# Kernel optimization log

Hardware: AMD Instinct MI355X
Metric: run time of the kernel (lower is better)

The kernel has to match this reference:

```python
import jax, jax.numpy as jnp
import numpy as np


def _apply_ring(x, angles):
    """Apply x @ R^T where R = G_0 @ G_1 @ ... @ G_{n-1} with ring planes
    (k, (k+1) % n). Equivalent to applying G_k^T to x for k = n-1 .. 0:
      x[:, k] <- c*x[:, k] - s*x[:, j]
      x[:, j] <- s*x[:, k] + c*x[:, j]
    x: [B, n], angles: [n].
    """
    n = angles.shape[0]

    def step(xT, k):
        a = angles[k]
        c, s = jnp.cos(a), jnp.sin(a)
        j = jnp.mod(k + 1, n)
        xi = xT[k]
        xj = xT[j]
        xT = xT.at[k].set(c * xi - s * xj)
        xT = xT.at[j].set(s * xi + c * xj)
        return xT, None

    ks = jnp.arange(n - 1, -1, -1)  # reverse order: R^T = G_{n-1}^T ... G_0^T
    xT, _ = jax.lax.scan(step, x.T, ks)  # carry is [n, B]
    return xT.T


def setup_inputs() -> dict:
    key = jax.random.key(0)
    k_x, k_e, k_d = jax.random.split(key, 3)
    B, n, num_blocks = 8192, 1024, 4
    return {
        "x": jax.random.normal(k_x, (B, n), dtype=jnp.float32),
        "angles_enc": jax.random.normal(k_e, (num_blocks, n), dtype=jnp.float32),
        "angles_dec": jax.random.normal(k_d, (num_blocks, n), dtype=jnp.float32),
        "hidden_weight": jnp.zeros((1,), dtype=jnp.float32),
        "hidden_state": jnp.zeros((n,), dtype=jnp.float32),
    }


def reference(x, angles_enc, angles_dec, hidden_weight, hidden_state):
    num_blocks = angles_enc.shape[0]
    b = x
    for blk in range(num_blocks):
        b = _apply_ring(b, angles_enc[blk])
    # recurrent blend; weight uses the detached hidden_weight (original uses
    # numpy on .detach()), so stop_gradient matches the original semantics.
    w = jax.nn.sigmoid(jax.lax.stop_gradient(hidden_weight[0]))
    bottleneck = (1.0 - w) * b + w * hidden_state[None, :]
    out = bottleneck
    for blk in range(num_blocks):
        out = _apply_ring(out, angles_dec[blk])
    return (bottleneck, out)
```

## Files before the change

kernel.cpp:

```cpp
#include <hip/hip_runtime.h>
#include <math.h>

#define N_COLS 1024
#define NRINGS 8

#define TPR    32
#define CHUNK  32
#define ROWS_PER_BLOCK 8

#define F_OFF   16384
#define A_OFF   24576
#define AUX_OFF 24832
#define WS_FLOATS 24848

__global__ __launch_bounds__(256)
void ced_setup(const float* __restrict__ ae,
               const float* __restrict__ ad,
               float* __restrict__ ws)
{
    __shared__ float2 ls[N_COLS];
    const int r   = blockIdx.x;
    const int tid = threadIdx.x;
    const float* ang = (r < 4) ? (ae + (r << 10)) : (ad + ((r - 4) << 10));

    #pragma unroll
    for (int m = 0; m < 4; ++m) {
        int k = (m << 8) + tid;
        float sv, cv;
        sincosf(ang[k], &sv, &cv);
        if (k == N_COLS - 1) {
            ((float2*)(ws + AUX_OFF))[r] = make_float2(cv, sv);
            cv = 0.f; sv = -1.f;
        }
        ls[k] = make_float2(cv, sv);
    }
    __syncthreads();

    const int t = tid >> 3;
    const int q = tid & 7;
    const int j0 = t * CHUNK + 4 * q;
    float2 e0 = ls[j0], e1 = ls[j0+1], e2 = ls[j0+2], e3 = ls[j0+3];

    float4* CSw = (float4*)ws;
    CSw[(r*16 + 2*q    )*32 + t] = make_float4(e0.x, e0.y, e1.x, e1.y);
    CSw[(r*16 + 2*q + 1)*32 + t] = make_float4(e2.x, e2.y, e3.x, e3.y);

    float f3 = e3.x;       float P = -e3.y;
    float f2 = e2.x * P;   P *= -e2.y;
    float f1 = e1.x * P;   P *= -e1.y;
    float f0 = e0.x * P;   P *= -e0.y;

    float ip = P;
    #pragma unroll
    for (int d = 1; d < 8; d <<= 1) {
        float tmp = __shfl_down(ip, d);
        if (q + d < 8) ip *= tmp;
    }
    float ex = __shfl_down(ip, 1);
    if (q == 7) ex = 1.f;
    f0 *= ex; f1 *= ex; f2 *= ex; f3 *= ex;

    float4* Fw = (float4*)(ws + F_OFF);
    Fw[(r*8 + q)*32 + t] = make_float4(f0, f1, f2, f3);
    if (q == 0) ws[A_OFF + r*TPR + t] = ip;
}

__global__ __launch_bounds__(256, 4)
void ced_main(const float* __restrict__ x,
              const float* __restrict__ ws,
              const float* __restrict__ hw,
              const float* __restrict__ hs,
              float* __restrict__ out, int B)
{
    const float4* CS  = (const float4*)ws;
    const float4* F   = (const float4*)(ws + F_OFF);
    const float*  A   = ws + A_OFF;
    const float2* AUX = (const float2*)(ws + AUX_OFF);

    const int tid  = threadIdx.x;
    const int lane = tid & 63;
    const int t    = lane & 31;
    const int g    = lane >> 5;
    const int groupBase = lane & 32;
    const int row  = blockIdx.x * ROWS_PER_BLOCK + (tid >> 6) * 2 + g;

    float y[CHUNK];
    const float4* xp = (const float4*)(x + (size_t)row * N_COLS + t * CHUNK);
    #pragma unroll
    for (int i = 0; i < 8; ++i) {
        float4 v = xp[i];
        y[4*i] = v.x; y[4*i+1] = v.y; y[4*i+2] = v.z; y[4*i+3] = v.w;
    }

    const float w   = 1.f / (1.f + expf(-hw[0]));
    const float omw = 1.f - w;

    #pragma unroll 1
    for (int r = 0; r < NRINGS; ++r) {
        if (r == 4) {
            float4* ob = (float4*)(out + (size_t)row * N_COLS + t * CHUNK);
            const float4* hp = (const float4*)(hs + t * CHUNK);
            #pragma unroll
            for (int i = 0; i < 8; ++i) {
                float4 h = hp[i];
                float4 bn;
                bn.x = fmaf(omw, y[4*i+0], w * h.x);
                bn.y = fmaf(omw, y[4*i+1], w * h.y);
                bn.z = fmaf(omw, y[4*i+2], w * h.z);
                bn.w = fmaf(omw, y[4*i+3], w * h.w);
                ob[i] = bn;
                y[4*i+0] = bn.x; y[4*i+1] = bn.y; y[4*i+2] = bn.z; y[4*i+3] = bn.w;
            }
        }

        const float4* csr = CS + r * 512 + t;
        float4 cs_all[16];
        #pragma unroll
        for (int jp = 0; jp < 16; ++jp) cs_all[jp] = csr[jp * 32];

        const float2 cN = AUX[r];
        float y0 = __shfl(y[0],       groupBase);
        float yN = __shfl(y[CHUNK-1], groupBase + 31);
        float Cinit = cN.x * yN - cN.y * y0;
        float x0n   = fmaf(cN.y, yN, cN.x * y0);
        if (t == 0) y[0] = x0n;

        float carry = 0.f, ztmp = 0.f;
        #pragma unroll
        for (int jp = CHUNK/2 - 1; jp >= 0; --jp) {
            float4 cs4 = cs_all[jp];
            const int j1 = 2*jp + 1;
            float z1 = fmaf(cs4.w, y[j1], cs4.z * carry);
            carry    = fmaf(-cs4.w, carry, cs4.z * y[j1]);
            if (j1 == CHUNK - 1) ztmp = z1; else y[j1+1] = z1;
            const int j0 = 2*jp;
            float z0s = fmaf(cs4.y, y[j0], cs4.x * carry);
            carry     = fmaf(-cs4.y, carry, cs4.x * y[j0]);
            y[j0+1] = z0s;
        }

        const float4* fr = F + r * 256 + t;
        float4 f_all[8];
        #pragma unroll
        for (int qi = 0; qi < 8; ++qi) f_all[qi] = fr[qi * 32];

        float sa = A[r*32 + t];
        float sb = carry;
        #pragma unroll
        for (int d = 1; d < TPR; d <<= 1) {
            float a2 = __shfl_down(sa, d);
            float b2 = __shfl_down(sb, d);
            if (t + d < TPR) { sb = fmaf(sa, b2, sb); sa *= a2; }
        }
        float ea = __shfl_down(sa, 1), eb = __shfl_down(sb, 1);
        float zfirst = fmaf(sa, Cinit, sb);
        float Cin = (t == TPR - 1) ? Cinit : fmaf(ea, Cinit, eb);

        #pragma unroll
        for (int qi = CHUNK/4 - 1; qi >= 0; --qi) {
            float4 f4 = f_all[qi];
            const int j = 4*qi;
            if (j + 3 == CHUNK - 1) ztmp   = fmaf(f4.w, Cin, ztmp);
            else                    y[j+4] = fmaf(f4.w, Cin, y[j+4]);
            y[j+3] = fmaf(f4.z, Cin, y[j+3]);
            y[j+2] = fmaf(f4.y, Cin, y[j+2]);
            y[j+1] = fmaf(f4.x, Cin, y[j+1]);
        }

        float up = __shfl_up(ztmp, 1);
        y[0] = (t == 0) ? zfirst : up;
    }

    float4* oo = (float4*)(out + (size_t)B * N_COLS + (size_t)row * N_COLS + t * CHUNK);
    #pragma unroll
    for (int i = 0; i < 8; ++i)
        oo[i] = make_float4(y[4*i], y[4*i+1], y[4*i+2], y[4*i+3]);
}

__global__ __launch_bounds__(256, 2)
void ced_fallback(const float* __restrict__ x,
                  const float* __restrict__ ae,
                  const float* __restrict__ ad,
                  const float* __restrict__ hw,
                  const float* __restrict__ hs,
                  float* __restrict__ out, int B)
{
    __shared__ float2 s_cs[NRINGS * 64 * 16];
    __shared__ float  s_A [NRINGS * 16];
    __shared__ float2 s_aux[NRINGS];

    const int tid = threadIdx.x;
    for (int i = 0; i < 32; ++i) {
        int idx = i * 256 + tid;
        int r   = idx >> 10;
        int k   = idx & 1023;
        const float* ang = (r < 4) ? (ae + (r << 10)) : (ad + ((r - 4) << 10));
        float sv, cv;
        sincosf(ang[k], &sv, &cv);
        int t = k >> 6, j = k & 63;
        float2 e = make_float2(cv, sv);
        if (k == 1023) { s_aux[r] = e; e = make_float2(0.f, -1.f); }
        s_cs[(r * 64 + j) * 16 + t] = e;
    }
    __syncthreads();
    if (tid < NRINGS * 16) {
        int r = tid >> 4, t = tid & 15;
        float p = 1.f;
        for (int j = 0; j < 64; ++j) p *= -s_cs[(r * 64 + j) * 16 + t].y;
        s_A[tid] = p;
    }
    __syncthreads();

    const int lane      = tid & 63;
    const int g         = lane >> 4;
    const int t         = lane & 15;
    const int groupBase = lane & 48;
    const int row       = blockIdx.x * 16 + (tid >> 6) * 4 + g;

    const float* xr = x + (size_t)row * N_COLS + t * 64;
    float y[64];
    #pragma unroll
    for (int i = 0; i < 16; ++i) {
        float4 v = ((const float4*)xr)[i];
        y[4*i] = v.x; y[4*i+1] = v.y; y[4*i+2] = v.z; y[4*i+3] = v.w;
    }
    const float w   = 1.f / (1.f + expf(-hw[0]));
    const float omw = 1.f - w;

    for (int r = 0; r < NRINGS; ++r) {
        if (r == 4) {
            float4* ob = (float4*)(out + (size_t)row * N_COLS + t * 64);
            const float4* hp = (const float4*)(hs + t * 64);
            #pragma unroll
            for (int i = 0; i < 16; ++i) {
                float4 h = hp[i];
                float4 bn;
                bn.x = fmaf(omw, y[4*i+0], w * h.x);
                bn.y = fmaf(omw, y[4*i+1], w * h.y);
                bn.z = fmaf(omw, y[4*i+2], w * h.z);
                bn.w = fmaf(omw, y[4*i+3], w * h.w);
                ob[i] = bn;
                y[4*i+0] = bn.x; y[4*i+1] = bn.y; y[4*i+2] = bn.z; y[4*i+3] = bn.w;
            }
        }
        const float2* csr = s_cs + r * 64 * 16;
        const float2  cN  = s_aux[r];
        float y0 = __shfl(y[0],  groupBase);
        float yN = __shfl(y[63], groupBase + 15);
        float Cinit = cN.x * yN - cN.y * y0;
        float x0n   = fmaf(cN.y, yN, cN.x * y0);
        if (t == 0) y[0] = x0n;

        float carry = 0.f, ztmp = 0.f;
        #pragma unroll
        for (int j = 63; j >= 0; --j) {
            float2 cs = csr[j * 16 + t];
            float z   = fmaf(cs.y, y[j], cs.x * carry);
            carry     = fmaf(-cs.y, carry, cs.x * y[j]);
            if (j == 63) ztmp = z; else y[j + 1] = z;
        }
        float sa = s_A[r * 16 + t], sb = carry;
        #pragma unroll
        for (int d = 1; d < 16; d <<= 1) {
            float a2 = __shfl_down(sa, d);
            float b2 = __shfl_down(sb, d);
            if (t + d < 16) { sb = fmaf(sa, b2, sb); sa *= a2; }
        }
        float ea = __shfl_down(sa, 1);
        float eb = __shfl_down(sb, 1);
        float z0  = fmaf(sa, Cinit, sb);
        float Cin = (t == 15) ? Cinit : fmaf(ea, Cinit, eb);

        float P = 1.f;
        #pragma unroll
        for (int j = 63; j >= 0; --j) {
            float2 cs = csr[j * 16 + t];
            float f = cs.x * P;
            P = -cs.y * P;
            if (j == 63) ztmp = fmaf(f, Cin, ztmp);
            else         y[j + 1] = fmaf(f, Cin, y[j + 1]);
        }
        float up = __shfl_up(ztmp, 1);
        y[0] = (t == 0) ? z0 : up;
    }

    float4* oo = (float4*)(out + (size_t)B * N_COLS + (size_t)row * N_COLS + t * 64);
    #pragma unroll
    for (int i = 0; i < 16; ++i)
        oo[i] = make_float4(y[4*i], y[4*i+1], y[4*i+2], y[4*i+3]);
}

extern "C" void kernel_launch(void* const* d_in, const int* in_sizes, int n_in,
                              void* d_out, int out_size, void* d_ws, size_t ws_size,
                              hipStream_t stream) {
    const float* x  = (const float*)d_in[0];
    const float* ae = (const float*)d_in[1];
    const float* ad = (const float*)d_in[2];
    const float* hw = (const float*)d_in[3];
    const float* hs = (const float*)d_in[4];
    float* out = (float*)d_out;
    const int B = in_sizes[0] / N_COLS;

    if (ws_size >= WS_FLOATS * sizeof(float)) {
        hipLaunchKernelGGL(ced_setup, dim3(NRINGS), dim3(256), 0, stream,
                           ae, ad, (float*)d_ws);
        hipLaunchKernelGGL(ced_main, dim3(B / ROWS_PER_BLOCK), dim3(256), 0, stream,
                           x, (const float*)d_ws, hw, hs, out, B);
    } else {
        hipLaunchKernelGGL(ced_fallback, dim3(B / 16), dim3(256), 0, stream,
                           x, ae, ad, hw, hs, out, B);
    }
}
```

Before: 137.5 us.

## Process two rows per thread group to reuse ring coefficients and interleave chains

The main kernel now has each 32-thread group hold two rows in registers, so each coefficient load (cs, F, A) and each scan step serves two independent recurrences. The two serial carry chains are interleaved to expose instruction-level parallelism, and occupancy hints drop from 4 to 2 blocks per CU to make room for the doubled register footprint. The setup kernel is split across 32 blocks instead of 8 to spread the sincos and prefix work. The trade is higher register pressure and fewer waves in flight, in exchange for more ILP and fewer redundant coefficient loads.

```diff
diff --git a/kernel.cpp b/kernel.cpp
--- a/kernel.cpp
+++ b/kernel.cpp
@@ -6,7 +6,7 @@
 
 #define TPR    32
 #define CHUNK  32
-#define ROWS_PER_BLOCK 8
+#define PAIRS_PER_BLOCK 8
 
 #define F_OFF   16384
 #define A_OFF   24576
@@ -18,54 +18,57 @@
                const float* __restrict__ ad,
                float* __restrict__ ws)
 {
-    __shared__ float2 ls[N_COLS];
-    const int r   = blockIdx.x;
+    __shared__ float2 ls[256];
+    const int r   = blockIdx.x >> 2;
+    const int b   = blockIdx.x & 3;
     const int tid = threadIdx.x;
+    const int k   = (b << 8) + tid;
     const float* ang = (r < 4) ? (ae + (r << 10)) : (ad + ((r - 4) << 10));
 
-    #pragma unroll
-    for (int m = 0; m < 4; ++m) {
-        int k = (m << 8) + tid;
-        float sv, cv;
-        sincosf(ang[k], &sv, &cv);
-        if (k == N_COLS - 1) {
-            ((float2*)(ws + AUX_OFF))[r] = make_float2(cv, sv);
-            cv = 0.f; sv = -1.f;
-        }
-        ls[k] = make_float2(cv, sv);
-    }
+    float sv, cv;
+    sincosf(ang[k], &sv, &cv);
+    if (k == N_COLS - 1) {
+        ((float2*)(ws + AUX_OFF))[r] = make_float2(cv, sv);
+        cv = 0.f; sv = -1.f;
+    }
+    ls[tid] = make_float2(cv, sv);
     __syncthreads();
 
-    const int t = tid >> 3;
-    const int q = tid & 7;
-    const int j0 = t * CHUNK + 4 * q;
-    float2 e0 = ls[j0], e1 = ls[j0+1], e2 = ls[j0+2], e3 = ls[j0+3];
-
-    float4* CSw = (float4*)ws;
-    CSw[(r*16 + 2*q    )*32 + t] = make_float4(e0.x, e0.y, e1.x, e1.y);
-    CSw[(r*16 + 2*q + 1)*32 + t] = make_float4(e2.x, e2.y, e3.x, e3.y);
-
-    float f3 = e3.x;       float P = -e3.y;
-    float f2 = e2.x * P;   P *= -e2.y;
-    float f1 = e1.x * P;   P *= -e1.y;
-    float f0 = e0.x * P;   P *= -e0.y;
-
-    float ip = P;
-    #pragma unroll
-    for (int d = 1; d < 8; d <<= 1) {
-        float tmp = __shfl_down(ip, d);
-        if (q + d < 8) ip *= tmp;
-    }
-    float ex = __shfl_down(ip, 1);
-    if (q == 7) ex = 1.f;
-    f0 *= ex; f1 *= ex; f2 *= ex; f3 *= ex;
-
-    float4* Fw = (float4*)(ws + F_OFF);
-    Fw[(r*8 + q)*32 + t] = make_float4(f0, f1, f2, f3);
-    if (q == 0) ws[A_OFF + r*TPR + t] = ip;
+    if (!(tid & 1)) {
+        float2 e0 = ls[tid], e1 = ls[tid + 1];
+        int t  = k >> 5;
+        int jp = (k & 31) >> 1;
+        ((float4*)ws)[(r*16 + jp)*32 + t] = make_float4(e0.x, e0.y, e1.x, e1.y);
+    }
+
+    if (tid < 64) {
+        const int lt = tid >> 3;
+        const int q  = tid & 7;
+        const int t  = (b << 3) + lt;
+        const int j0 = lt * CHUNK + 4 * q;
+        float2 e0 = ls[j0], e1 = ls[j0+1], e2 = ls[j0+2], e3 = ls[j0+3];
+
+        float f3 = e3.x;       float P = -e3.y;
+        float f2 = e2.x * P;   P *= -e2.y;
+        float f1 = e1.x * P;   P *= -e1.y;
+        float f0 = e0.x * P;   P *= -e0.y;
+
+        float ip = P;
+        #pragma unroll
+        for (int d = 1; d < 8; d <<= 1) {
+            float tmp = __shfl_down(ip, d);
+            if (q + d < 8) ip *= tmp;
+        }
+        float ex = __shfl_down(ip, 1);
+        if (q == 7) ex = 1.f;
+        f0 *= ex; f1 *= ex; f2 *= ex; f3 *= ex;
+
+        ((float4*)(ws + F_OFF))[(r*8 + q)*32 + t] = make_float4(f0, f1, f2, f3);
+        if (q == 0) ws[A_OFF + r*TPR + t] = ip;
+    }
 }
 
-__global__ __launch_bounds__(256, 4)
+__global__ __launch_bounds__(256, 2)
 void ced_main(const float* __restrict__ x,
               const float* __restrict__ ws,
               const float* __restrict__ hw,
@@ -80,16 +83,22 @@
     const int tid  = threadIdx.x;
     const int lane = tid & 63;
     const int t    = lane & 31;
-    const int g    = lane >> 5;
     const int groupBase = lane & 32;
-    const int row  = blockIdx.x * ROWS_PER_BLOCK + (tid >> 6) * 2 + g;
-
-    float y[CHUNK];
-    const float4* xp = (const float4*)(x + (size_t)row * N_COLS + t * CHUNK);
-    #pragma unroll
-    for (int i = 0; i < 8; ++i) {
-        float4 v = xp[i];
-        y[4*i] = v.x; y[4*i+1] = v.y; y[4*i+2] = v.z; y[4*i+3] = v.w;
+    const int pair = blockIdx.x * PAIRS_PER_BLOCK + (tid >> 5);
+
+    const size_t rowA = (size_t)(2 * pair) * N_COLS;
+    const size_t rowB = rowA + N_COLS;
+
+    float ya[CHUNK], yb[CHUNK];
+    {
+        const float4* xa = (const float4*)(x + rowA + t * CHUNK);
+        const float4* xb = (const float4*)(x + rowB + t * CHUNK);
+        #pragma unroll
+        for (int i = 0; i < 8; ++i) {
+            float4 va = xa[i], vb = xb[i];
+            ya[4*i] = va.x; ya[4*i+1] = va.y; ya[4*i+2] = va.z; ya[4*i+3] = va.w;
+            yb[4*i] = vb.x; yb[4*i+1] = vb.y; yb[4*i+2] = vb.z; yb[4*i+3] = vb.w;
+        }
     }
 
     const float w   = 1.f / (1.f + expf(-hw[0]));
@@ -98,18 +107,24 @@
     #pragma unroll 1
     for (int r = 0; r < NRINGS; ++r) {
         if (r == 4) {
-            float4* ob = (float4*)(out + (size_t)row * N_COLS + t * CHUNK);
+            float4* oa = (float4*)(out + rowA + t * CHUNK);
+            float4* ob = (float4*)(out + rowB + t * CHUNK);
             const float4* hp = (const float4*)(hs + t * CHUNK);
             #pragma unroll
             for (int i = 0; i < 8; ++i) {
                 float4 h = hp[i];
-                float4 bn;
-                bn.x = fmaf(omw, y[4*i+0], w * h.x);
-                bn.y = fmaf(omw, y[4*i+1], w * h.y);
-                bn.z = fmaf(omw, y[4*i+2], w * h.z);
-                bn.w = fmaf(omw, y[4*i+3], w * h.w);
-                ob[i] = bn;
-                y[4*i+0] = bn.x; y[4*i+1] = bn.y; y[4*i+2] = bn.z; y[4*i+3] = bn.w;
+                float4 na, nb;
+                na.x = fmaf(omw, ya[4*i+0], w * h.x);
+                na.y = fmaf(omw, ya[4*i+1], w * h.y);
+                na.z = fmaf(omw, ya[4*i+2], w * h.z);
+                na.w = fmaf(omw, ya[4*i+3], w * h.w);
+                nb.x = fmaf(omw, yb[4*i+0], w * h.x);
+                nb.y = fmaf(omw, yb[4*i+1], w * h.y);
+                nb.z = fmaf(omw, yb[4*i+2], w * h.z);
+                nb.w = fmaf(omw, yb[4*i+3], w * h.w);
+                oa[i] = na; ob[i] = nb;
+                ya[4*i+0] = na.x; ya[4*i+1] = na.y; ya[4*i+2] = na.z; ya[4*i+3] = na.w;
+                yb[4*i+0] = nb.x; yb[4*i+1] = nb.y; yb[4*i+2] = nb.z; yb[4*i+3] = nb.w;
             }
         }
 
@@ -119,24 +134,33 @@
         for (int jp = 0; jp < 16; ++jp) cs_all[jp] = csr[jp * 32];
 
         const float2 cN = AUX[r];
-        float y0 = __shfl(y[0],       groupBase);
-        float yN = __shfl(y[CHUNK-1], groupBase + 31);
-        float Cinit = cN.x * yN - cN.y * y0;
-        float x0n   = fmaf(cN.y, yN, cN.x * y0);
-        if (t == 0) y[0] = x0n;
-
-        float carry = 0.f, ztmp = 0.f;
+        float y0a = __shfl(ya[0],       groupBase);
+        float yNa = __shfl(ya[CHUNK-1], groupBase + 31);
+        float y0b = __shfl(yb[0],       groupBase);
+        float yNb = __shfl(yb[CHUNK-1], groupBase + 31);
+        float CinitA = cN.x * yNa - cN.y * y0a;
+        float CinitB = cN.x * yNb - cN.y * y0b;
+        float x0nA   = fmaf(cN.y, yNa, cN.x * y0a);
+        float x0nB   = fmaf(cN.y, yNb, cN.x * y0b);
+        if (t == 0) { ya[0] = x0nA; yb[0] = x0nB; }
+
+        float carA = 0.f, carB = 0.f, ztA = 0.f, ztB = 0.f;
         #pragma unroll
         for (int jp = CHUNK/2 - 1; jp >= 0; --jp) {
             float4 cs4 = cs_all[jp];
             const int j1 = 2*jp + 1;
-            float z1 = fmaf(cs4.w, y[j1], cs4.z * carry);
-            carry    = fmaf(-cs4.w, carry, cs4.z * y[j1]);
-            if (j1 == CHUNK - 1) ztmp = z1; else y[j1+1] = z1;
+            float z1a = fmaf(cs4.w, ya[j1], cs4.z * carA);
+            float z1b = fmaf(cs4.w, yb[j1], cs4.z * carB);
+            carA = fmaf(-cs4.w, carA, cs4.z * ya[j1]);
+            carB = fmaf(-cs4.w, carB, cs4.z * yb[j1]);
+            if (j1 == CHUNK - 1) { ztA = z1a; ztB = z1b; }
+            else                 { ya[j1+1] = z1a; yb[j1+1] = z1b; }
             const int j0 = 2*jp;
-            float z0s = fmaf(cs4.y, y[j0], cs4.x * carry);
-            carry     = fmaf(-cs4.y, carry, cs4.x * y[j0]);
-            y[j0+1] = z0s;
+            float z0a = fmaf(cs4.y, ya[j0], cs4.x * carA);
+            float z0b = fmaf(cs4.y, yb[j0], cs4.x * carB);
+            carA = fmaf(-cs4.y, carA, cs4.x * ya[j0]);
+            carB = fmaf(-cs4.y, carB, cs4.x * yb[j0]);
+            ya[j0+1] = z0a; yb[j0+1] = z0b;
         }
 
         const float4* fr = F + r * 256 + t;
@@ -145,36 +169,52 @@
         for (int qi = 0; qi < 8; ++qi) f_all[qi] = fr[qi * 32];
 
         float sa = A[r*32 + t];
-        float sb = carry;
+        float sbA = carA, sbB = carB;
         #pragma unroll
         for (int d = 1; d < TPR; d <<= 1) {
-            float a2 = __shfl_down(sa, d);
-            float b2 = __shfl_down(sb, d);
-            if (t + d < TPR) { sb = fmaf(sa, b2, sb); sa *= a2; }
-        }
-        float ea = __shfl_down(sa, 1), eb = __shfl_down(sb, 1);
-        float zfirst = fmaf(sa, Cinit, sb);
-        float Cin = (t == TPR - 1) ? Cinit : fmaf(ea, Cinit, eb);
+            float a2  = __shfl_down(sa,  d);
+            float b2a = __shfl_down(sbA, d);
+            float b2b = __shfl_down(sbB, d);
+            if (t + d < TPR) {
+                sbA = fmaf(sa, b2a, sbA);
+                sbB = fmaf(sa, b2b, sbB);
+                sa *= a2;
+            }
+        }
+        float ea  = __shfl_down(sa,  1);
+        float ebA = __shfl_down(sbA, 1);
+        float ebB = __shfl_down(sbB, 1);
+        float zfA = fmaf(sa, CinitA, sbA);
+        float zfB = fmaf(sa, CinitB, sbB);
+        float CinA = (t == TPR - 1) ? CinitA : fmaf(ea, CinitA, ebA);
+        float CinB = (t == TPR - 1) ? CinitB : fmaf(ea, CinitB, ebB);
 
         #pragma unroll
         for (int qi = CHUNK/4 - 1; qi >= 0; --qi) {
             float4 f4 = f_all[qi];
             const int j = 4*qi;
-            if (j + 3 == CHUNK - 1) ztmp   = fmaf(f4.w, Cin, ztmp);
-            else                    y[j+4] = fmaf(f4.w, Cin, y[j+4]);
-            y[j+3] = fmaf(f4.z, Cin, y[j+3]);
-            y[j+2] = fmaf(f4.y, Cin, y[j+2]);
-            y[j+1] = fmaf(f4.x, Cin, y[j+1]);
-        }
-
-        float up = __shfl_up(ztmp, 1);
-        y[0] = (t == 0) ? zfirst : up;
-    }
-
-    float4* oo = (float4*)(out + (size_t)B * N_COLS + (size_t)row * N_COLS + t * CHUNK);
+            if (j + 3 == CHUNK - 1) { ztA = fmaf(f4.w, CinA, ztA);
+                                      ztB = fmaf(f4.w, CinB, ztB); }
+            else                    { ya[j+4] = fmaf(f4.w, CinA, ya[j+4]);
+                                      yb[j+4] = fmaf(f4.w, CinB, yb[j+4]); }
+            ya[j+3] = fmaf(f4.z, CinA, ya[j+3]);  yb[j+3] = fmaf(f4.z, CinB, yb[j+3]);
+            ya[j+2] = fmaf(f4.y, CinA, ya[j+2]);  yb[j+2] = fmaf(f4.y, CinB, yb[j+2]);
+            ya[j+1] = fmaf(f4.x, CinA, ya[j+1]);  yb[j+1] = fmaf(f4.x, CinB, yb[j+1]);
+        }
+
+        float upA = __shfl_up(ztA, 1);
+        float upB = __shfl_up(ztB, 1);
+        ya[0] = (t == 0) ? zfA : upA;
+        yb[0] = (t == 0) ? zfB : upB;
+    }
+
+    float4* oa = (float4*)(out + (size_t)B * N_COLS + rowA + t * CHUNK);
+    float4* ob = (float4*)(out + (size_t)B * N_COLS + rowB + t * CHUNK);
     #pragma unroll
-    for (int i = 0; i < 8; ++i)
-        oo[i] = make_float4(y[4*i], y[4*i+1], y[4*i+2], y[4*i+3]);
+    for (int i = 0; i < 8; ++i) {
+        oa[i] = make_float4(ya[4*i], ya[4*i+1], ya[4*i+2], ya[4*i+3]);
+        ob[i] = make_float4(yb[4*i], yb[4*i+1], yb[4*i+2], yb[4*i+3]);
+    }
 }
 
 __global__ __launch_bounds__(256, 2)
@@ -302,9 +342,9 @@
     const int B = in_sizes[0] / N_COLS;
 
     if (ws_size >= WS_FLOATS * sizeof(float)) {
-        hipLaunchKernelGGL(ced_setup, dim3(NRINGS), dim3(256), 0, stream,
+        hipLaunchKernelGGL(ced_setup, dim3(32), dim3(256), 0, stream,
                            ae, ad, (float*)d_ws);
-        hipLaunchKernelGGL(ced_main, dim3(B / ROWS_PER_BLOCK), dim3(256), 0, stream,
+        hipLaunchKernelGGL(ced_main, dim3(B / (2 * PAIRS_PER_BLOCK)), dim3(256), 0, stream,
                            x, (const float*)d_ws, hw, hs, out, B);
     } else {
         hipLaunchKernelGGL(ced_fallback, dim3(B / 16), dim3(256), 0, stream,
```

Result: no change. 136.7 us (-0.6%).
